# Optimization experiments

Hardware: AMD Instinct MI355X
Metric: run time of the kernel (lower is better)

## Reference

```python
import jax, jax.numpy as jnp
import numpy as np

B, T, D, DFF, E = 4, 2048, 1024, 4096, 8


def setup_inputs() -> dict:
    key = jax.random.key(0)
    ks = jax.random.split(key, 4)
    s_in = 1.0 / np.sqrt(D)
    s_ff = 1.0 / np.sqrt(DFF)
    return {
        "x": jax.random.normal(ks[0], (B, T, D), dtype=jnp.float32),
        "gate_W": jax.random.normal(ks[1], (D, E), dtype=jnp.float32) * s_in,
        "gate_b": jnp.zeros((E,), dtype=jnp.float32),
        "W1": jax.random.normal(ks[2], (E, D, DFF), dtype=jnp.float32) * s_in,
        "b1": jnp.zeros((E, DFF), dtype=jnp.float32),
        "W2": jax.random.normal(ks[3], (E, DFF, D), dtype=jnp.float32) * s_ff,
        "b2": jnp.zeros((E, D), dtype=jnp.float32),
    }


def reference(x, gate_W, gate_b, W1, b1, W2, b2):
    # x: [B, T, D]. Top-1 gated MoE; each expert FFN runs on the (masked)
    # full token set, exactly as the original dense-masked implementation.
    b, t, d = x.shape
    num_experts = gate_W.shape[-1]
    logits = jnp.einsum("btd,de->bte", x, gate_W) + gate_b  # [B,T,E]
    top1 = jnp.argmax(logits, axis=-1).reshape(-1)          # [B*T]
    flat_x = x.reshape(b * t, d)                            # [N,D]
    out = jnp.zeros_like(flat_x)
    for e in range(num_experts):  # small fixed expert count
        mask = (top1 == e).astype(x.dtype)[:, None]         # [N,1]
        h = jax.nn.gelu((flat_x * mask) @ W1[e] + b1[e], approximate=False)
        out = out + (h @ W2[e] + b2[e]) * mask
    return out.reshape(b, t, d)
```

## Files before the change

### kernel.cpp

```cpp
#include <hip/hip_runtime.h>
#include <hip/hip_bf16.h>
#include <cstdint>

#define N_TOK 8192
#define D_IN  1024
#define DFF   4096
#define NE    8
#define DEPTH 3

typedef __bf16 bf16x8 __attribute__((ext_vector_type(8)));
typedef float  f32x4  __attribute__((ext_vector_type(4)));

__device__ __forceinline__ unsigned short f2bf(float f) {
  unsigned u = __float_as_uint(f);
  u += 0x7fffu + ((u >> 16) & 1u);
  return (unsigned short)(u >> 16);
}

__device__ __forceinline__ void gll16(const void* g, void* l) {
  __builtin_amdgcn_global_load_lds(
      (__attribute__((address_space(1))) void*)g,
      (__attribute__((address_space(3))) void*)l, 16, 0, 0);
}

__global__ __launch_bounds__(256) void gate_kernel(
    const float* __restrict__ x, const float* __restrict__ gW,
    const float* __restrict__ gb, unsigned short* __restrict__ xbf,
    int* __restrict__ top1) {
  int wave = threadIdx.x >> 6, lane = threadIdx.x & 63;
  int n = blockIdx.x * 4 + wave;
  const float* xr = x + (size_t)n * D_IN;
  double acc[NE];
#pragma unroll
  for (int e = 0; e < NE; ++e) acc[e] = 0.0;
#pragma unroll
  for (int j = 0; j < 16; ++j) {
    int d = j * 64 + lane;
    float v = xr[d];
    xbf[(size_t)n * D_IN + d] = f2bf(v);
    float4 g0 = *(const float4*)(gW + (size_t)d * 8);
    float4 g1 = *(const float4*)(gW + (size_t)d * 8 + 4);
    acc[0] += (double)v * (double)g0.x;
    acc[1] += (double)v * (double)g0.y;
    acc[2] += (double)v * (double)g0.z;
    acc[3] += (double)v * (double)g0.w;
    acc[4] += (double)v * (double)g1.x;
    acc[5] += (double)v * (double)g1.y;
    acc[6] += (double)v * (double)g1.z;
    acc[7] += (double)v * (double)g1.w;
  }
#pragma unroll
  for (int m = 32; m >= 1; m >>= 1) {
#pragma unroll
    for (int e = 0; e < NE; ++e) acc[e] += __shfl_xor(acc[e], m);
  }
  if (lane == 0) {
    float best = (float)acc[0] + gb[0];
    int be = 0;
#pragma unroll
    for (int e = 1; e < NE; ++e) {
      float lv = (float)acc[e] + gb[e];
      if (lv > best) { best = lv; be = e; }
    }
    top1[n] = be;
  }
}

__global__ __launch_bounds__(1024) void build_kernel(
    const int* __restrict__ top1, int* __restrict__ hdr, int* __restrict__ perm,
    int* __restrict__ tile_e, int* __restrict__ tile_m, int* __restrict__ sub0) {
  __shared__ int cnt[NE];
  int tid = threadIdx.x;
  if (tid < NE) cnt[tid] = 0;
  __syncthreads();
  int mye[8], myp[8];
#pragma unroll
  for (int r = 0; r < 8; ++r) {
    int n = r * 1024 + tid;
    int e = top1[n];
    mye[r] = e;
    myp[r] = atomicAdd(&cnt[e], 1);
  }
  __syncthreads();
  if (tid == 0) {
    int o = 0;
    int n1 = 0, n2 = 0;
    for (int e = 0; e < NE; ++e) {
      int Me = cnt[e];
      hdr[e] = Me;
      hdr[8 + e] = o;
      o += Me;
    }
    hdr[16] = o;
    for (int e = 0; e < NE; ++e) {
      int Me = cnt[e];
      int base2 = n2;
      n2 += (Me + 63) >> 6;
      for (int m0 = 0; m0 < Me; m0 += 128) {
        tile_e[n1] = e; tile_m[n1] = m0; sub0[n1] = base2 + (m0 >> 6); ++n1;
      }
    }
    hdr[17] = n1;
    hdr[18] = n2;
  }
  __syncthreads();
#pragma unroll
  for (int r = 0; r < 8; ++r) {
    int n = r * 1024 + tid;
    perm[mye[r] * N_TOK + myp[r]] = n;
  }
}

__global__ __launch_bounds__(256) void apack_kernel(
    const unsigned short* __restrict__ xbf, const int* __restrict__ hdr,
    const int* __restrict__ tile_e, const int* __restrict__ tile_m,
    const int* __restrict__ perm, unsigned short* __restrict__ Apack) {
  int wi = blockIdx.x >> 2;
  if (wi >= hdr[17]) return;
  int q = blockIdx.x & 3;
  int e = tile_e[wi], m0 = tile_m[wi], Me = hdr[e];
  int wave = threadIdx.x >> 6, lane = threadIdx.x & 63;
  int kq = lane >> 4, m = lane & 15;
#pragma unroll
  for (int s = 0; s < 2; ++s) {
    int g = wave * 2 + s;
    int r = m0 + g * 16 + m;
    if (r >= Me) r = Me - 1;
    int token = perm[e * N_TOK + r];
    const char* src = (const char*)xbf + (size_t)token * 2048 + kq * 16;
    char* dst = (char*)Apack + (size_t)wi * 32 * 8192 + g * 1024 + lane * 16;
    for (int kk = 0; kk < 8; ++kk)
      *(int4*)(dst + (size_t)(q * 8 + kk) * 8192) = *(const int4*)(src + (q * 8 + kk) * 64);
  }
}

__device__ __forceinline__ void wpack_body(
    const float* __restrict__ src, unsigned short* __restrict__ dst,
    int R, int C, int tiles_r, int tiles_c, int bid) {
  __shared__ unsigned short tile[64][72];
  int tpe = tiles_r * tiles_c;
  int e = bid / tpe;
  int t = bid % tpe;
  int r0 = (t / tiles_c) * 64, c0 = (t % tiles_c) * 64;
  const float* s = src + (size_t)e * R * C;
  int tr = threadIdx.x >> 4, tc = (threadIdx.x & 15) * 4;
#pragma unroll
  for (int p = 0; p < 4; ++p) {
    int row = r0 + tr + p * 16;
    const float4 v = *(const float4*)(s + (size_t)row * C + c0 + tc);
    tile[tc + 0][tr + p * 16] = f2bf(v.x);
    tile[tc + 1][tr + p * 16] = f2bf(v.y);
    tile[tc + 2][tr + p * 16] = f2bf(v.z);
    tile[tc + 3][tr + p * 16] = f2bf(v.w);
  }
  __syncthreads();
  int nkk = R >> 5, ntc = C >> 7;
#pragma unroll
  for (int u = 0; u < 2; ++u) {
    int c = u * 256 + threadIdx.x;
    int kk_l = c >> 8, gg_l = (c >> 6) & 3, kq = (c >> 4) & 3, mm = c & 15;
    int fl = gg_l * 16 + mm;
    int kl = kk_l * 32 + kq * 8;
    int4 val = *(const int4*)&tile[fl][kl];
    int f = c0 + fl;
    int nt = f >> 7, gg = (f >> 4) & 7;
    int kk = (r0 >> 5) + kk_l;
    size_t off = ((((size_t)e * ntc + nt) * nkk + kk) * 8 + gg) * 1024 + (kq * 16 + mm) * 16;
    *(int4*)((char*)dst + off) = val;
  }
}

__global__ __launch_bounds__(256) void wpack_both(
    const float* __restrict__ W1, unsigned short* __restrict__ B1,
    const float* __restrict__ W2, unsigned short* __restrict__ B2) {
  if (blockIdx.x < NE * 16 * 64)
    wpack_body(W1, B1, D_IN, DFF, 16, 64, blockIdx.x);
  else
    wpack_body(W2, B2, DFF, D_IN, 64, 16, blockIdx.x - NE * 16 * 64);
}

__global__ __launch_bounds__(256) void gemm1(
    const unsigned short* __restrict__ Apack, const unsigned short* __restrict__ Bpack1,
    const float* __restrict__ b1, const int* __restrict__ hdr,
    const int* __restrict__ tile_e, const int* __restrict__ tile_m,
    const int* __restrict__ sub0, unsigned short* __restrict__ Hpack) {
  int wi = blockIdx.x >> 5;
  if (wi >= hdr[17]) return;
  int nt = blockIdx.x & 31;
  int e = tile_e[wi];
  int m0 = tile_m[wi];
  int Me = hdr[e];
  int n0 = nt * 128;

  __shared__ __align__(16) char smem[49152];
  char* Asm = smem;
  char* Bsm = smem + 24576;

  int tid = threadIdx.x, wave = tid >> 6, lane = tid & 63;
  int wm = wave >> 1, wn = wave & 1;

  const char* abase = (const char*)Apack + (size_t)wi * 32 * 8192;
  const char* bbase = (const char*)Bpack1 + (size_t)(e * 32 + nt) * 32 * 8192;
  int off0 = (wave * 2 + 0) * 1024 + lane * 16;
  int off1 = (wave * 2 + 1) * 1024 + lane * 16;

  const int NITER = D_IN / 32;
#pragma unroll
  for (int p = 0; p < DEPTH; ++p) {
    gll16(abase + (size_t)p * 8192 + off0, Asm + p * 8192 + off0);
    gll16(abase + (size_t)p * 8192 + off1, Asm + p * 8192 + off1);
    gll16(bbase + (size_t)p * 8192 + off0, Bsm + p * 8192 + off0);
    gll16(bbase + (size_t)p * 8192 + off1, Bsm + p * 8192 + off1);
  }

  f32x4 acc[4][4];
#pragma unroll
  for (int i = 0; i < 4; ++i)
#pragma unroll
    for (int j = 0; j < 4; ++j) { f32x4 z = {0.f, 0.f, 0.f, 0.f}; acc[i][j] = z; }

  int cur = 0;
  for (int kk = 0; kk < NITER; ++kk) {
    asm volatile("s_waitcnt vmcnt(8)" ::: "memory");
    __builtin_amdgcn_s_barrier();
    const char* ab = Asm + cur * 8192;
    const char* bb = Bsm + cur * 8192;
    bf16x8 af[4], bfv[4];
#pragma unroll
    for (int i = 0; i < 4; ++i)
      af[i] = *(const bf16x8*)(ab + (wm * 4 + i) * 1024 + lane * 16);
#pragma unroll
    for (int j = 0; j < 4; ++j)
      bfv[j] = *(const bf16x8*)(bb + (wn * 4 + j) * 1024 + lane * 16);
    asm volatile("s_waitcnt lgkmcnt(0)" ::: "memory");
    __builtin_amdgcn_s_barrier();
    int nx = kk + DEPTH;
    if (nx > NITER - 1) nx = NITER - 1;
    char* ad = Asm + cur * 8192;
    char* bd = Bsm + cur * 8192;
    gll16(abase + (size_t)nx * 8192 + off0, ad + off0);
    gll16(abase + (size_t)nx * 8192 + off1, ad + off1);
    gll16(bbase + (size_t)nx * 8192 + off0, bd + off0);
    gll16(bbase + (size_t)nx * 8192 + off1, bd + off1);
#pragma unroll
    for (int i = 0; i < 4; ++i)
#pragma unroll
      for (int j = 0; j < 4; ++j)
        acc[i][j] = __builtin_amdgcn_mfma_f32_16x16x32_bf16(af[i], bfv[j], acc[i][j], 0, 0, 0);
    cur = (cur == DEPTH - 1) ? 0 : cur + 1;
  }

  asm volatile("s_waitcnt vmcnt(0)" ::: "memory");
  __syncthreads();
  unsigned short* Cl = (unsigned short*)smem;
  int quad = lane >> 4, col_l = lane & 15;
#pragma unroll
  for (int i = 0; i < 4; ++i) {
#pragma unroll
    for (int j = 0; j < 4; ++j) {
      int f = n0 + wn * 64 + j * 16 + col_l;
      float bb = b1[(size_t)e * DFF + f];
      int lc = wn * 64 + j * 16 + col_l;
#pragma unroll
      for (int r = 0; r < 4; ++r) {
        int lr = wm * 64 + i * 16 + quad * 4 + r;
        float v = acc[i][j][r] + bb;
        v = 0.5f * v * (1.0f + erff(v * 0.70710678118654752f));
        Cl[lr * 128 + lc] = f2bf(v);
      }
    }
  }
  __syncthreads();
  int s0 = sub0[wi];
  bool hasB = (m0 + 64 < Me);
#pragma unroll
  for (int u = 0; u < 8; ++u) {
    int c = u * 256 + tid;
    int lr = c >> 4, fc = c & 15;
    int sv = lr >> 6;
    if (sv == 1 && !hasB) continue;
    int4 val = *(const int4*)(Cl + lr * 128 + fc * 8);
    int wi2 = s0 + sv;
    int m2 = lr & 63;
    int gg = m2 >> 4, mm = m2 & 15;
    int kk2 = nt * 4 + (fc >> 2), kq2 = fc & 3;
    *(int4*)((char*)Hpack + ((size_t)wi2 * 128 + kk2) * 4096 + gg * 1024 + (kq2 * 16 + mm) * 16) = val;
  }
}

__global__ __launch_bounds__(256) void gemm2(
    const unsigned short* __restrict__ Hpack, const unsigned short* __restrict__ Bpack2,
    const float* __restrict__ b2, const int* __restrict__ hdr,
    const int* __restrict__ tile_e, const int* __restrict__ tile_m,
    const int* __restrict__ sub0, const int* __restrict__ perm,
    float* __restrict__ out) {
  int wi = blockIdx.x >> 3;
  if (wi >= hdr[17]) return;
  int nt = blockIdx.x & 7;
  int e = tile_e[wi];
  int m0 = tile_m[wi];
  int Me = hdr[e];
  int n0 = nt * 128;
  int s0 = sub0[wi];
  int s1 = (m0 + 64 < Me) ? s0 + 1 : s0;

  __shared__ __align__(16) char smem[49152];
  char* Asm = smem;
  char* Bsm = smem + 24576;

  int tid = threadIdx.x, wave = tid >> 6, lane = tid & 63;
  int wm = wave >> 1, wn = wave & 1;

  const char* abase_s[2];
  int agl[2];
  int off_s[2];
#pragma unroll
  for (int s = 0; s < 2; ++s) {
    int g = wave * 2 + s;
    int sv = g >> 2;
    abase_s[s] = (const char*)Hpack + (size_t)((sv ? s1 : s0) * 128) * 4096;
    agl[s] = (g & 3) * 1024 + lane * 16;
    off_s[s] = g * 1024 + lane * 16;
  }
  const char* bbase = (const char*)Bpack2 + (size_t)(e * 8 + nt) * 128 * 8192;

  const int NITER = DFF / 32;
#pragma unroll
  for (int p = 0; p < DEPTH; ++p) {
    gll16(abase_s[0] + (size_t)p * 4096 + agl[0], Asm + p * 8192 + off_s[0]);
    gll16(abase_s[1] + (size_t)p * 4096 + agl[1], Asm + p * 8192 + off_s[1]);
    gll16(bbase + (size_t)p * 8192 + off_s[0], Bsm + p * 8192 + off_s[0]);
    gll16(bbase + (size_t)p * 8192 + off_s[1], Bsm + p * 8192 + off_s[1]);
  }

  f32x4 acc[4][4];
#pragma unroll
  for (int i = 0; i < 4; ++i)
#pragma unroll
    for (int j = 0; j < 4; ++j) { f32x4 z = {0.f, 0.f, 0.f, 0.f}; acc[i][j] = z; }

  int cur = 0;
  for (int kk = 0; kk < NITER; ++kk) {
    asm volatile("s_waitcnt vmcnt(8)" ::: "memory");
    __builtin_amdgcn_s_barrier();
    const char* ab = Asm + cur * 8192;
    const char* bb = Bsm + cur * 8192;
    bf16x8 af[4], bfv[4];
#pragma unroll
    for (int i = 0; i < 4; ++i)
      af[i] = *(const bf16x8*)(ab + (wm * 4 + i) * 1024 + lane * 16);
#pragma unroll
    for (int j = 0; j < 4; ++j)
      bfv[j] = *(const bf16x8*)(bb + (wn * 4 + j) * 1024 + lane * 16);
    asm volatile("s_waitcnt lgkmcnt(0)" ::: "memory");
    __builtin_amdgcn_s_barrier();
    int nx = kk + DEPTH;
    if (nx > NITER - 1) nx = NITER - 1;
    char* ad = Asm + cur * 8192;
    char* bd = Bsm + cur * 8192;
    gll16(abase_s[0] + (size_t)nx * 4096 + agl[0], ad + off_s[0]);
    gll16(abase_s[1] + (size_t)nx * 4096 + agl[1], ad + off_s[1]);
    gll16(bbase + (size_t)nx * 8192 + off_s[0], bd + off_s[0]);
    gll16(bbase + (size_t)nx * 8192 + off_s[1], bd + off_s[1]);
#pragma unroll
    for (int i = 0; i < 4; ++i)
#pragma unroll
      for (int j = 0; j < 4; ++j)
        acc[i][j] = __builtin_amdgcn_mfma_f32_16x16x32_bf16(af[i], bfv[j], acc[i][j], 0, 0, 0);
    cur = (cur == DEPTH - 1) ? 0 : cur + 1;
  }

  int quad = lane >> 4, col_l = lane & 15;
#pragma unroll
  for (int i = 0; i < 4; ++i) {
    int rbase = m0 + wm * 64 + i * 16 + quad * 4;
#pragma unroll
    for (int j = 0; j < 4; ++j) {
      int col = n0 + wn * 64 + j * 16 + col_l;
      float bb = b2[(size_t)e * D_IN + col];
#pragma unroll
      for (int r = 0; r < 4; ++r) {
        int rr = rbase + r;
        if (rr < Me) {
          int token = perm[e * N_TOK + rr];
          out[(size_t)token * D_IN + col] = acc[i][j][r] + bb;
        }
      }
    }
  }
}

extern "C" void kernel_launch(void* const* d_in, const int* in_sizes, int n_in,
                              void* d_out, int out_size, void* d_ws, size_t ws_size,
                              hipStream_t stream) {
  const float* x  = (const float*)d_in[0];
  const float* gW = (const float*)d_in[1];
  const float* gb = (const float*)d_in[2];
  const float* W1 = (const float*)d_in[3];
  const float* b1 = (const float*)d_in[4];
  const float* W2 = (const float*)d_in[5];
  const float* b2 = (const float*)d_in[6];
  float* out = (float*)d_out;

  char* ws = (char*)d_ws;
  int* hdr     = (int*)ws;
  int* tile_e  = (int*)(ws + 4096);
  int* tile_m  = (int*)(ws + 4608);
  int* sub0    = (int*)(ws + 5120);
  int* top1    = (int*)(ws + 8192);
  int* perm    = (int*)(ws + 65536);
  unsigned short* xbf    = (unsigned short*)(ws + 524288);
  unsigned short* Bpack2 = (unsigned short*)(ws + 524288);
  unsigned short* Apack  = (unsigned short*)(ws + 69206016);
  unsigned short* Bpack1 = (unsigned short*)(ws + 92274688);
  unsigned short* Hpack  = (unsigned short*)(ws + 159383552);

  gate_kernel<<<N_TOK / 4, 256, 0, stream>>>(x, gW, gb, xbf, top1);
  build_kernel<<<1, 1024, 0, stream>>>(top1, hdr, perm, tile_e, tile_m, sub0);
  apack_kernel<<<71 * 4, 256, 0, stream>>>(xbf, hdr, tile_e, tile_m, perm, Apack);
  wpack_both<<<NE * 16 * 64 + NE * 64 * 16, 256, 0, stream>>>(W1, Bpack1, W2, Bpack2);
  gemm1<<<71 * 32, 256, 0, stream>>>(Apack, Bpack1, b1, hdr, tile_e, tile_m, sub0, Hpack);
  gemm2<<<71 * 8, 256, 0, stream>>>(Hpack, Bpack2, b2, hdr, tile_e, tile_m, sub0, perm, out);
}
```

Baseline: 567.3 us.

## Enlarge GEMM1 tiles to 256x256 with 512-thread blocks and repacked operands

Replaces the 128x128 first expert GEMM with a 256x256 tile version using 8 waves, double-buffered LDS staging and setprio around the MFMA block. A and W1 are repacked into a matching 256-wide layout, and build_kernel emits a 256-row tile list. Bigger tiles raise arithmetic intensity and cut redundant global loads, at the cost of more padding waste on partial expert tiles, more registers per thread and a shallower prefetch pipeline.

```diff
diff --git a/kernel.cpp b/kernel.cpp
--- a/kernel.cpp
+++ b/kernel.cpp
@@ -7,6 +7,7 @@
 #define DFF   4096
 #define NE    8
 #define DEPTH 3
+#define MAXT256 40
 
 typedef __bf16 bf16x8 __attribute__((ext_vector_type(8)));
 typedef float  f32x4  __attribute__((ext_vector_type(4)));
@@ -68,7 +69,8 @@
 
 __global__ __launch_bounds__(1024) void build_kernel(
     const int* __restrict__ top1, int* __restrict__ hdr, int* __restrict__ perm,
-    int* __restrict__ tile_e, int* __restrict__ tile_m, int* __restrict__ sub0) {
+    int* __restrict__ tile_e, int* __restrict__ tile_m, int* __restrict__ sub0,
+    int* __restrict__ t256_e, int* __restrict__ t256_m, int* __restrict__ t256_s) {
   __shared__ int cnt[NE];
   int tid = threadIdx.x;
   if (tid < NE) cnt[tid] = 0;
@@ -84,7 +86,7 @@
   __syncthreads();
   if (tid == 0) {
     int o = 0;
-    int n1 = 0, n2 = 0;
+    int n1 = 0, n2 = 0, n256 = 0;
     for (int e = 0; e < NE; ++e) {
       int Me = cnt[e];
       hdr[e] = Me;
@@ -99,9 +101,13 @@
       for (int m0 = 0; m0 < Me; m0 += 128) {
         tile_e[n1] = e; tile_m[n1] = m0; sub0[n1] = base2 + (m0 >> 6); ++n1;
       }
+      for (int m0 = 0; m0 < Me; m0 += 256) {
+        t256_e[n256] = e; t256_m[n256] = m0; t256_s[n256] = base2 + (m0 >> 6); ++n256;
+      }
     }
     hdr[17] = n1;
     hdr[18] = n2;
+    hdr[19] = n256;
   }
   __syncthreads();
 #pragma unroll
@@ -111,26 +117,64 @@
   }
 }
 
-__global__ __launch_bounds__(256) void apack_kernel(
+__global__ __launch_bounds__(256) void apack256_kernel(
     const unsigned short* __restrict__ xbf, const int* __restrict__ hdr,
-    const int* __restrict__ tile_e, const int* __restrict__ tile_m,
+    const int* __restrict__ t256_e, const int* __restrict__ t256_m,
     const int* __restrict__ perm, unsigned short* __restrict__ Apack) {
-  int wi = blockIdx.x >> 2;
-  if (wi >= hdr[17]) return;
-  int q = blockIdx.x & 3;
-  int e = tile_e[wi], m0 = tile_m[wi], Me = hdr[e];
-  int wave = threadIdx.x >> 6, lane = threadIdx.x & 63;
+  int ti = blockIdx.x >> 3;
+  if (ti >= hdr[19]) return;
+  int part = blockIdx.x & 7;
+  int h = part >> 2, ktq = part & 3;
+  int e = t256_e[ti], m0 = t256_m[ti], Me = hdr[e];
+  int w = threadIdx.x >> 6, lane = threadIdx.x & 63;
   int kq = lane >> 4, m = lane & 15;
 #pragma unroll
-  for (int s = 0; s < 2; ++s) {
-    int g = wave * 2 + s;
-    int r = m0 + g * 16 + m;
+  for (int g2 = 0; g2 < 2; ++g2) {
+    int g = w * 2 + g2;
+    int r = m0 + h * 128 + g * 16 + m;
     if (r >= Me) r = Me - 1;
     int token = perm[e * N_TOK + r];
     const char* src = (const char*)xbf + (size_t)token * 2048 + kq * 16;
-    char* dst = (char*)Apack + (size_t)wi * 32 * 8192 + g * 1024 + lane * 16;
-    for (int kk = 0; kk < 8; ++kk)
-      *(int4*)(dst + (size_t)(q * 8 + kk) * 8192) = *(const int4*)(src + (q * 8 + kk) * 64);
+    char* dst = (char*)Apack + (size_t)ti * 524288 + h * 8192 + g * 1024 + lane * 16;
+#pragma unroll
+    for (int kt2 = 0; kt2 < 8; ++kt2) {
+      int kt = ktq * 8 + kt2;
+      *(int4*)(dst + (size_t)kt * 16384) = *(const int4*)(src + kt * 64);
+    }
+  }
+}
+
+__device__ __forceinline__ void wpack_w1_body(
+    const float* __restrict__ src, unsigned short* __restrict__ dst, int bid) {
+  __shared__ unsigned short tile[64][72];
+  int e = bid >> 10;
+  int t = bid & 1023;
+  int r0 = (t >> 6) * 64, c0 = (t & 63) * 64;
+  const float* s = src + (size_t)e * D_IN * DFF;
+  int tr = threadIdx.x >> 4, tc = (threadIdx.x & 15) * 4;
+#pragma unroll
+  for (int p = 0; p < 4; ++p) {
+    int row = r0 + tr + p * 16;
+    const float4 v = *(const float4*)(s + (size_t)row * DFF + c0 + tc);
+    tile[tc + 0][tr + p * 16] = f2bf(v.x);
+    tile[tc + 1][tr + p * 16] = f2bf(v.y);
+    tile[tc + 2][tr + p * 16] = f2bf(v.z);
+    tile[tc + 3][tr + p * 16] = f2bf(v.w);
+  }
+  __syncthreads();
+#pragma unroll
+  for (int u = 0; u < 2; ++u) {
+    int c = u * 256 + threadIdx.x;
+    int kk_l = c >> 8, gg_l = (c >> 6) & 3, kq = (c >> 4) & 3, mm = c & 15;
+    int fl = gg_l * 16 + mm;
+    int kl = kk_l * 32 + kq * 8;
+    int4 val = *(const int4*)&tile[fl][kl];
+    int f = c0 + fl;
+    int nt = f >> 8, h = (f >> 7) & 1, g = (f >> 4) & 7;
+    int kt = (r0 >> 5) + kk_l;
+    size_t off = ((size_t)(e * 16 + nt) * 32 + kt) * 16384 +
+                 (size_t)h * 8192 + g * 1024 + (kq * 16 + mm) * 16;
+    *(int4*)((char*)dst + off) = val;
   }
 }
 
@@ -174,117 +218,124 @@
     const float* __restrict__ W1, unsigned short* __restrict__ B1,
     const float* __restrict__ W2, unsigned short* __restrict__ B2) {
   if (blockIdx.x < NE * 16 * 64)
-    wpack_body(W1, B1, D_IN, DFF, 16, 64, blockIdx.x);
+    wpack_w1_body(W1, B1, blockIdx.x);
   else
     wpack_body(W2, B2, DFF, D_IN, 64, 16, blockIdx.x - NE * 16 * 64);
 }
 
-__global__ __launch_bounds__(256) void gemm1(
+__global__ __launch_bounds__(512, 2) void gemm1_256(
     const unsigned short* __restrict__ Apack, const unsigned short* __restrict__ Bpack1,
     const float* __restrict__ b1, const int* __restrict__ hdr,
-    const int* __restrict__ tile_e, const int* __restrict__ tile_m,
-    const int* __restrict__ sub0, unsigned short* __restrict__ Hpack) {
-  int wi = blockIdx.x >> 5;
-  if (wi >= hdr[17]) return;
-  int nt = blockIdx.x & 31;
-  int e = tile_e[wi];
-  int m0 = tile_m[wi];
-  int Me = hdr[e];
-  int n0 = nt * 128;
-
-  __shared__ __align__(16) char smem[49152];
-  char* Asm = smem;
-  char* Bsm = smem + 24576;
+    const int* __restrict__ t256_e, const int* __restrict__ t256_m,
+    const int* __restrict__ t256_s, unsigned short* __restrict__ Hpack) {
+  int ti = blockIdx.x >> 4;
+  if (ti >= hdr[19]) return;
+  int nt = blockIdx.x & 15;
+  int e = t256_e[ti], m0 = t256_m[ti], Me = hdr[e];
+  int n0 = nt * 256;
+
+  __shared__ __align__(16) char smem[65536];
 
   int tid = threadIdx.x, wave = tid >> 6, lane = tid & 63;
-  int wm = wave >> 1, wn = wave & 1;
-
-  const char* abase = (const char*)Apack + (size_t)wi * 32 * 8192;
-  const char* bbase = (const char*)Bpack1 + (size_t)(e * 32 + nt) * 32 * 8192;
-  int off0 = (wave * 2 + 0) * 1024 + lane * 16;
-  int off1 = (wave * 2 + 1) * 1024 + lane * 16;
+  int wm = wave >> 2, wn = wave & 3;
+
+  const char* aBase = (const char*)Apack + (size_t)ti * 524288;
+  const char* bBase = (const char*)Bpack1 + (size_t)(e * 16 + nt) * 524288;
+
+  auto stage = [&](int kt) {
+    int b = kt & 1;
+    const char* sB = bBase + (size_t)kt * 16384 + tid * 16;
+    char* dB = smem + 32768 + b * 16384 + tid * 16;
+    gll16(sB, dB);
+    gll16(sB + 8192, dB + 8192);
+    const char* sA = aBase + (size_t)kt * 16384 + tid * 16;
+    char* dA = smem + b * 16384 + tid * 16;
+    gll16(sA, dA);
+    gll16(sA + 8192, dA + 8192);
+  };
+
+  stage(0);
+  stage(1);
+
+  f32x4 acc[8][4];
+#pragma unroll
+  for (int i = 0; i < 8; ++i)
+#pragma unroll
+    for (int j = 0; j < 4; ++j) { f32x4 z = {0.f, 0.f, 0.f, 0.f}; acc[i][j] = z; }
 
   const int NITER = D_IN / 32;
-#pragma unroll
-  for (int p = 0; p < DEPTH; ++p) {
-    gll16(abase + (size_t)p * 8192 + off0, Asm + p * 8192 + off0);
-    gll16(abase + (size_t)p * 8192 + off1, Asm + p * 8192 + off1);
-    gll16(bbase + (size_t)p * 8192 + off0, Bsm + p * 8192 + off0);
-    gll16(bbase + (size_t)p * 8192 + off1, Bsm + p * 8192 + off1);
-  }
-
-  f32x4 acc[4][4];
-#pragma unroll
-  for (int i = 0; i < 4; ++i)
-#pragma unroll
-    for (int j = 0; j < 4; ++j) { f32x4 z = {0.f, 0.f, 0.f, 0.f}; acc[i][j] = z; }
-
-  int cur = 0;
-  for (int kk = 0; kk < NITER; ++kk) {
-    asm volatile("s_waitcnt vmcnt(8)" ::: "memory");
+  for (int T = 0; T < NITER; ++T) {
+    int b = T & 1;
+    asm volatile("s_waitcnt vmcnt(4)" ::: "memory");
     __builtin_amdgcn_s_barrier();
-    const char* ab = Asm + cur * 8192;
-    const char* bb = Bsm + cur * 8192;
-    bf16x8 af[4], bfv[4];
-#pragma unroll
-    for (int i = 0; i < 4; ++i)
-      af[i] = *(const bf16x8*)(ab + (wm * 4 + i) * 1024 + lane * 16);
-#pragma unroll
-    for (int j = 0; j < 4; ++j)
-      bfv[j] = *(const bf16x8*)(bb + (wn * 4 + j) * 1024 + lane * 16);
+    const char* Ap = smem + b * 16384 + wm * 8192 + lane * 16;
+    const char* Bp = smem + 32768 + b * 16384 + (wn >> 1) * 8192 + (wn & 1) * 4096 + lane * 16;
+    bf16x8 a[8], bf[4];
+#pragma unroll
+    for (int i = 0; i < 8; ++i) a[i] = *(const bf16x8*)(Ap + i * 1024);
+#pragma unroll
+    for (int j = 0; j < 4; ++j) bf[j] = *(const bf16x8*)(Bp + j * 1024);
     asm volatile("s_waitcnt lgkmcnt(0)" ::: "memory");
+    __builtin_amdgcn_sched_barrier(0);
     __builtin_amdgcn_s_barrier();
-    int nx = kk + DEPTH;
+    int nx = T + 2;
     if (nx > NITER - 1) nx = NITER - 1;
-    char* ad = Asm + cur * 8192;
-    char* bd = Bsm + cur * 8192;
-    gll16(abase + (size_t)nx * 8192 + off0, ad + off0);
-    gll16(abase + (size_t)nx * 8192 + off1, ad + off1);
-    gll16(bbase + (size_t)nx * 8192 + off0, bd + off0);
-    gll16(bbase + (size_t)nx * 8192 + off1, bd + off1);
-#pragma unroll
-    for (int i = 0; i < 4; ++i)
+    stage(nx);
+    __builtin_amdgcn_s_setprio(1);
+#pragma unroll
+    for (int i = 0; i < 8; ++i)
 #pragma unroll
       for (int j = 0; j < 4; ++j)
-        acc[i][j] = __builtin_amdgcn_mfma_f32_16x16x32_bf16(af[i], bfv[j], acc[i][j], 0, 0, 0);
-    cur = (cur == DEPTH - 1) ? 0 : cur + 1;
+        acc[i][j] = __builtin_amdgcn_mfma_f32_16x16x32_bf16(a[i], bf[j], acc[i][j], 0, 0, 0);
+    __builtin_amdgcn_s_setprio(0);
   }
 
   asm volatile("s_waitcnt vmcnt(0)" ::: "memory");
   __syncthreads();
   unsigned short* Cl = (unsigned short*)smem;
   int quad = lane >> 4, col_l = lane & 15;
-#pragma unroll
-  for (int i = 0; i < 4; ++i) {
-#pragma unroll
-    for (int j = 0; j < 4; ++j) {
-      int f = n0 + wn * 64 + j * 16 + col_l;
-      float bb = b1[(size_t)e * DFF + f];
-      int lc = wn * 64 + j * 16 + col_l;
-#pragma unroll
-      for (int r = 0; r < 4; ++r) {
-        int lr = wm * 64 + i * 16 + quad * 4 + r;
-        float v = acc[i][j][r] + bb;
-        v = 0.5f * v * (1.0f + erff(v * 0.70710678118654752f));
-        Cl[lr * 128 + lc] = f2bf(v);
+  float bb[4];
+#pragma unroll
+  for (int j = 0; j < 4; ++j)
+    bb[j] = b1[(size_t)e * DFF + n0 + wn * 64 + j * 16 + col_l];
+  int s0 = t256_s[ti];
+  int rem = Me - m0; if (rem > 256) rem = 256;
+  int nsv = (rem + 63) >> 6;
+#pragma unroll
+  for (int h = 0; h < 2; ++h) {
+    if (wm == h) {
+#pragma unroll
+      for (int i = 0; i < 8; ++i) {
+#pragma unroll
+        for (int j = 0; j < 4; ++j) {
+          int lc = wn * 64 + j * 16 + col_l;
+#pragma unroll
+          for (int r = 0; r < 4; ++r) {
+            int lr_l = i * 16 + quad * 4 + r;
+            float v = acc[i][j][r] + bb[j];
+            v = 0.5f * v * (1.0f + erff(v * 0.70710678118654752f));
+            Cl[lr_l * 256 + lc] = f2bf(v);
+          }
+        }
       }
     }
-  }
-  __syncthreads();
-  int s0 = sub0[wi];
-  bool hasB = (m0 + 64 < Me);
-#pragma unroll
-  for (int u = 0; u < 8; ++u) {
-    int c = u * 256 + tid;
-    int lr = c >> 4, fc = c & 15;
-    int sv = lr >> 6;
-    if (sv == 1 && !hasB) continue;
-    int4 val = *(const int4*)(Cl + lr * 128 + fc * 8);
-    int wi2 = s0 + sv;
-    int m2 = lr & 63;
-    int gg = m2 >> 4, mm = m2 & 15;
-    int kk2 = nt * 4 + (fc >> 2), kq2 = fc & 3;
-    *(int4*)((char*)Hpack + ((size_t)wi2 * 128 + kk2) * 4096 + gg * 1024 + (kq2 * 16 + mm) * 16) = val;
+    __syncthreads();
+#pragma unroll
+    for (int u = 0; u < 8; ++u) {
+      int c = u * 512 + tid;
+      int lr_l = c >> 5, fc = c & 31;
+      int lr = h * 128 + lr_l;
+      int sv = lr >> 6;
+      if (sv < nsv) {
+        int4 val = *(const int4*)(Cl + lr_l * 256 + fc * 8);
+        int wi2 = s0 + sv;
+        int m2 = lr & 63;
+        int gg = m2 >> 4, mm = m2 & 15;
+        int kk2 = nt * 8 + (fc >> 2), kq2 = fc & 3;
+        *(int4*)((char*)Hpack + ((size_t)wi2 * 128 + kk2) * 4096 + gg * 1024 + (kq2 * 16 + mm) * 16) = val;
+      }
+    }
+    __syncthreads();
   }
 }
 
@@ -407,6 +458,9 @@
   int* tile_e  = (int*)(ws + 4096);
   int* tile_m  = (int*)(ws + 4608);
   int* sub0    = (int*)(ws + 5120);
+  int* t256_e  = (int*)(ws + 5632);
+  int* t256_m  = (int*)(ws + 6144);
+  int* t256_s  = (int*)(ws + 6656);
   int* top1    = (int*)(ws + 8192);
   int* perm    = (int*)(ws + 65536);
   unsigned short* xbf    = (unsigned short*)(ws + 524288);
@@ -416,9 +470,11 @@
   unsigned short* Hpack  = (unsigned short*)(ws + 159383552);
 
   gate_kernel<<<N_TOK / 4, 256, 0, stream>>>(x, gW, gb, xbf, top1);
-  build_kernel<<<1, 1024, 0, stream>>>(top1, hdr, perm, tile_e, tile_m, sub0);
-  apack_kernel<<<71 * 4, 256, 0, stream>>>(xbf, hdr, tile_e, tile_m, perm, Apack);
+  build_kernel<<<1, 1024, 0, stream>>>(top1, hdr, perm, tile_e, tile_m, sub0,
+                                       t256_e, t256_m, t256_s);
+  apack256_kernel<<<MAXT256 * 8, 256, 0, stream>>>(xbf, hdr, t256_e, t256_m, perm, Apack);
   wpack_both<<<NE * 16 * 64 + NE * 64 * 16, 256, 0, stream>>>(W1, Bpack1, W2, Bpack2);
-  gemm1<<<71 * 32, 256, 0, stream>>>(Apack, Bpack1, b1, hdr, tile_e, tile_m, sub0, Hpack);
+  gemm1_256<<<MAXT256 * 16, 512, 0, stream>>>(Apack, Bpack1, b1, hdr,
+                                              t256_e, t256_m, t256_s, Hpack);
   gemm2<<<71 * 8, 256, 0, stream>>>(Hpack, Bpack2, b2, hdr, tile_e, tile_m, sub0, perm, out);
 }
```

New measurement: 677.8 us. +19.5%, slower.
